# Kernel optimization log

Hardware: AMD Instinct MI355X
Metric: run time of the kernel (lower is better)

Reference implementation:

```python
import jax, jax.numpy as jnp
import numpy as np

N_NODES = 100000
N_EDGES = 1600000
D_IN = 128
H1 = 128           # hidden_channels
H2 = int(H1 * 0.6) # 76, per int(hidden_channels * 0.6)
D_OUT = 64


def setup_inputs() -> dict:
    key = jax.random.key(0)
    ks = jax.random.split(key, 12)
    def lin(k, fan_in, fan_out):
        # torch Linear default init: U(-1/sqrt(fan_in), 1/sqrt(fan_in)); stored as [in, out]
        bound = 1.0 / np.sqrt(fan_in)
        return jax.random.uniform(k, (fan_in, fan_out), jnp.float32, -bound, bound)
    x = jax.random.normal(ks[0], (N_NODES, D_IN), jnp.float32)
    edge_index = jax.random.randint(ks[1], (2, N_EDGES), 0, N_NODES, dtype=jnp.int64)
    return {
        "x": x,
        "edge_index": edge_index,
        "Wl1": lin(ks[2], D_IN, H1),  "Wr1": lin(ks[3], D_IN, H1),
        "b1": jnp.zeros((H1,), jnp.float32),
        "Wl2": lin(ks[4], H1, H2),    "Wr2": lin(ks[5], H1, H2),
        "b2": jnp.zeros((H2,), jnp.float32),
        "Wl3": lin(ks[6], H2, D_OUT), "Wr3": lin(ks[7], H2, D_OUT),
        "b3": jnp.zeros((D_OUT,), jnp.float32),
    }


def reference(x, edge_index, Wl1, Wr1, b1, Wl2, Wr2, b2, Wl3, Wr3, b3):
    src, dst = edge_index[0], edge_index[1]
    n = x.shape[0]
    # in-degree of each target node (mean aggregation denominator), clamped to 1
    deg = jax.ops.segment_sum(jnp.ones_like(src, dtype=x.dtype), dst, num_segments=n)
    inv_deg = (1.0 / jnp.maximum(deg, 1.0))[:, None]

    def sage(h, Wl, Wr, b):
        # gather source features, scatter-add to targets, mean, then dual linear
        agg = jax.ops.segment_sum(h[src], dst, num_segments=n) * inv_deg
        return agg @ Wl + h @ Wr + b  # lin_l(mean_j x_j) + lin_r(x_i) + bias

    h = jax.nn.relu(sage(x, Wl1, Wr1, b1))
    h = jax.nn.relu(sage(h, Wl2, Wr2, b2))
    return sage(h, Wl3, Wr3, b3)
```

## Files before the change

### kernel.cpp

```cpp
#include <hip/hip_runtime.h>
#include <hip/hip_bf16.h>
#include <cstdint>
#include <cstddef>


typedef __attribute__((ext_vector_type(8))) short bf16x8;
typedef __attribute__((ext_vector_type(4))) float f32x4;

__device__ __forceinline__ short f2bf(float f) {
  uint32_t u = __builtin_bit_cast(uint32_t, f);
  u += 0x7fffu + ((u >> 16) & 1u);
  return (short)(u >> 16);
}
__device__ __forceinline__ float bflo(uint32_t u) {
  union { uint32_t i; float f; } v; v.i = u << 16; return v.f;
}
__device__ __forceinline__ float bfhi(uint32_t u) {
  union { uint32_t i; float f; } v; v.i = u & 0xffff0000u; return v.f;
}
__device__ __forceinline__ uint32_t pkbf(float a, float b) {
  return (uint32_t)(uint16_t)f2bf(a) | ((uint32_t)(uint16_t)f2bf(b) << 16);
}

__global__ void k_detect(const int* __restrict__ ei, int* __restrict__ flag, int E) {
  int t = threadIdx.x;
  int stride = E / 4096; if (stride < 1) stride = 1;
  int found = 0;
  for (int i = t; i < 4096; i += 256) {
    long long e = (long long)i * stride;
    if (e < E && ei[2 * e + 1] != 0) found = 1;
  }
  if (found) atomicOr(flag, 1);
}

__device__ __forceinline__ int edge_val(const int* ei, int is64, size_t pos) {
  return is64 ? ei[2 * pos] : ei[pos];
}

#define GPART 256

__global__ __launch_bounds__(256)
void k_bhist(const int* __restrict__ ei, const int* __restrict__ flag,
             int* __restrict__ hist, int E, int NB, int CPB) {
  __shared__ int lh[1024];
  int g = blockIdx.x, t = threadIdx.x;
  for (int b = t; b < NB; b += 256) lh[b] = 0;
  __syncthreads();
  int is64 = (*flag == 0);
  int e0 = g * CPB, e1 = min(e0 + CPB, E);
  for (int e = e0 + t; e < e1; e += 256) {
    int d = edge_val(ei, is64, (size_t)E + e);
    atomicAdd(&lh[d >> 7], 1);
  }
  __syncthreads();
  for (int b = t; b < NB; b += 256) hist[(size_t)g * NB + b] = lh[b];
}

__global__ void k_csum(const int* __restrict__ hist, int* __restrict__ total,
                       int NB, int G) {
  int b = blockIdx.x, t = threadIdx.x;
  int s = 0;
  for (int g = t; g < G; g += 64) s += hist[(size_t)g * NB + b];
  for (int off = 32; off; off >>= 1) s += __shfl_down(s, off);
  if (t == 0) total[b] = s;
}

__global__ void k_bscan(const int* __restrict__ total, int* __restrict__ bbase,
                        int NB) {
  __shared__ int sh[1024];
  int t = threadIdx.x;
  int v = (t < NB) ? total[t] : 0;
  sh[t] = v; __syncthreads();
  for (int off = 1; off < 1024; off <<= 1) {
    int x = (t >= off) ? sh[t - off] : 0;
    __syncthreads();
    sh[t] += x;
    __syncthreads();
  }
  if (t < NB) bbase[t] = sh[t] - v;
  if (t == NB - 1) bbase[NB] = sh[t];
}

__global__ void k_coff(int* __restrict__ hist, const int* __restrict__ bbase,
                       int NB, int G) {
  int b = blockIdx.x, t = threadIdx.x;
  int carry = bbase[b];
  for (int g0 = 0; g0 < G; g0 += 64) {
    int v = hist[(size_t)(g0 + t) * NB + b];
    int incl = v;
    #pragma unroll
    for (int off = 1; off < 64; off <<= 1) {
      int x = __shfl_up(incl, off);
      if (t >= off) incl += x;
    }
    hist[(size_t)(g0 + t) * NB + b] = carry + incl - v;
    carry += __shfl(incl, 63);
  }
}

__global__ __launch_bounds__(256)
void k_bscatter(const int* __restrict__ ei, const int* __restrict__ flag,
                const int* __restrict__ off, uint32_t* __restrict__ staging,
                int E, int NB, int CPB) {
  __shared__ int lcur[1024];
  int g = blockIdx.x, t = threadIdx.x;
  for (int b = t; b < NB; b += 256) lcur[b] = off[(size_t)g * NB + b];
  __syncthreads();
  int is64 = (*flag == 0);
  int e0 = g * CPB, e1 = min(e0 + CPB, E);
  for (int e = e0 + t; e < e1; e += 256) {
    int s = edge_val(ei, is64, (size_t)e);
    int d = edge_val(ei, is64, (size_t)E + e);
    int p = atomicAdd(&lcur[d >> 7], 1);
    staging[p] = ((uint32_t)(d & 127) << 25) | (uint32_t)s;
  }
}

#define LDSCAP 12288
__global__ __launch_bounds__(256)
void k_bfinal(const uint32_t* __restrict__ staging, const int* __restrict__ bbase,
              int* __restrict__ row_start, int* __restrict__ sorted_src,
              int N, int NB, int E) {
  __shared__ uint32_t ent[LDSCAP];
  __shared__ int cnt[128];
  __shared__ int pre[128];
  int b = blockIdx.x, t = threadIdx.x;
  int base = bbase[b], sz = bbase[b + 1] - base;
  int n0 = b << 7;
  if (t < 128) cnt[t] = 0;
  __syncthreads();
  bool fit = (sz <= LDSCAP);
  if (fit) {
    for (int i = t; i < sz; i += 256) {
      uint32_t u = staging[base + i];
      ent[i] = u;
      atomicAdd(&cnt[u >> 25], 1);
    }
  } else {
    for (int i = t; i < sz; i += 256)
      atomicAdd(&cnt[staging[base + i] >> 25], 1);
  }
  __syncthreads();
  if (t < 128) pre[t] = cnt[t];
  __syncthreads();
  #pragma unroll
  for (int off = 1; off < 128; off <<= 1) {
    int x = (t < 128 && t >= off) ? pre[t - off] : 0;
    __syncthreads();
    if (t < 128) pre[t] += x;
    __syncthreads();
  }
  int nn = N - n0; if (nn > 128) nn = 128;
  if (t < 128) {
    int ex = pre[t] - cnt[t];
    if (t < nn) row_start[n0 + t] = base + ex;
    cnt[t] = ex;
  }
  if (b == NB - 1 && t == 0) row_start[N] = E;
  __syncthreads();
  if (fit) {
    for (int i = t; i < sz; i += 256) {
      uint32_t u = ent[i];
      int p = atomicAdd(&cnt[u >> 25], 1);
      sorted_src[base + p] = (int)(u & 0x1FFFFFFu);
    }
  } else {
    for (int i = t; i < sz; i += 256) {
      uint32_t u = staging[base + i];
      int p = atomicAdd(&cnt[u >> 25], 1);
      sorted_src[base + p] = (int)(u & 0x1FFFFFFu);
    }
  }
}

__global__ void k_wprep(const float* __restrict__ Wl, const float* __restrict__ Wr,
                        short* __restrict__ Wt, int K, int H, int Hp, int Kp, int NP) {
  int idx = blockIdx.x * 256 + threadIdx.x;
  if (idx >= NP * Kp) return;
  int c = idx / Kp, k = idx - c * Kp;
  float v = 0.f;
  if (k < K) {
    if (c < H) v = Wl[(size_t)k * H + c];
    else if (c >= Hp && c - Hp < H) v = Wr[(size_t)k * H + (c - Hp)];
  }
  Wt[idx] = f2bf(v);
}

template<int MODE, int NKS, int QBF16, int MAXCF>
__global__ __launch_bounds__(256, 3)
void k_gemm3(const void* __restrict__ Av, const short* __restrict__ Wt,
             const float* __restrict__ bias, short* __restrict__ P,
             void* __restrict__ Qv, int M, int lda, int H, int Hp, int F) {
  constexpr int Kp = NKS * 32;
  constexpr int PKv = Kp + 8;
  __shared__ short As[64 * PKv];
  int t = threadIdx.x;
  int wv = __builtin_amdgcn_readfirstlane(t >> 6);
  int lane = t & 63;
  int l16 = lane & 15, lk8 = (lane >> 4) * 8;
  int m0 = blockIdx.x * 64;

  if (MODE == 0) {
    const float* A = (const float*)Av;
    #pragma unroll
    for (int i = 0; i < 8; i++) {
      int c = t + i * 256;
      int row = c >> 5, q = c & 31;
      int gr = m0 + row;
      float4 v = make_float4(0.f, 0.f, 0.f, 0.f);
      if (gr < M) v = *(const float4*)(A + (size_t)gr * lda + q * 4);
      uint2 pk; pk.x = pkbf(v.x, v.y); pk.y = pkbf(v.z, v.w);
      *(uint2*)&As[row * PKv + q * 4] = pk;
    }
  } else {
    const short* A = (const short*)Av;
    constexpr int cpr = Kp / 8;
    #pragma unroll
    for (int i = 0; i < (64 * cpr) / 256; i++) {
      int c = t + i * 256;
      int row = c / cpr, q = c - row * cpr;
      int gr = m0 + row;
      uint4 v = make_uint4(0u, 0u, 0u, 0u);
      if (gr < M) v = *(const uint4*)(A + (size_t)gr * lda + q * 8);
      *(uint4*)&As[row * PKv + q * 8] = v;
    }
  }

  bf16x8 b[MAXCF][NKS];
  float4 bia[MAXCF];
  int cbase[MAXCF];
  bool isPc[MAXCF];
  bool cok[MAXCF];
  bool fragUse[MAXCF];
  #pragma unroll
  for (int i = 0; i < MAXCF; i++) {
    int cfrag = wv + 4 * i;
    fragUse[i] = cfrag < F;
    bool p = cfrag * 16 < Hp;
    int cb = cfrag * 16 + ((lane >> 4) << 2) - (p ? 0 : Hp);
    cbase[i] = cb; isPc[i] = p;
    cok[i] = fragUse[i] && (cb < H);
    bia[i] = make_float4(0.f, 0.f, 0.f, 0.f);
    if (cok[i] && !p) bia[i] = *(const float4*)(bias + cb);
    if (fragUse[i]) {
      const short* wp = Wt + (size_t)(cfrag * 16 + l16) * Kp + lk8;
      #pragma unroll
      for (int ks = 0; ks < NKS; ks++)
        b[i][ks] = *(const bf16x8*)(wp + ks * 32);
    } else {
      #pragma unroll
      for (int ks = 0; ks < NKS; ks++)
        b[i][ks] = (bf16x8){0, 0, 0, 0, 0, 0, 0, 0};
    }
  }

  __syncthreads();

  #pragma unroll
  for (int rf = 0; rf < 4; rf++) {
    bf16x8 a[NKS];
    #pragma unroll
    for (int ks = 0; ks < NKS; ks++)
      a[ks] = *(const bf16x8*)&As[(rf * 16 + l16) * PKv + ks * 32 + lk8];

    f32x4 acc[MAXCF];
    #pragma unroll
    for (int i = 0; i < MAXCF; i++) acc[i] = (f32x4){0.f, 0.f, 0.f, 0.f};
    #pragma unroll
    for (int ks = 0; ks < NKS; ks++) {
      #pragma unroll
      for (int i = 0; i < MAXCF; i++) {
        if (fragUse[i])
          acc[i] = __builtin_amdgcn_mfma_f32_16x16x32_bf16(b[i][ks], a[ks], acc[i], 0, 0, 0);
      }
    }

    int node = m0 + rf * 16 + l16;
    if (node < M) {
      #pragma unroll
      for (int i = 0; i < MAXCF; i++) {
        if (cok[i]) {
          if (isPc[i]) {
            uint2 pk;
            pk.x = pkbf(acc[i][0], acc[i][1]);
            pk.y = pkbf(acc[i][2], acc[i][3]);
            *(uint2*)(P + (size_t)node * H + cbase[i]) = pk;
          } else if (QBF16) {
            uint2 pk;
            pk.x = pkbf(acc[i][0] + bia[i].x, acc[i][1] + bia[i].y);
            pk.y = pkbf(acc[i][2] + bia[i].z, acc[i][3] + bia[i].w);
            *(uint2*)((short*)Qv + (size_t)node * H + cbase[i]) = pk;
          } else {
            float4 r;
            r.x = acc[i][0] + bia[i].x; r.y = acc[i][1] + bia[i].y;
            r.z = acc[i][2] + bia[i].z; r.w = acc[i][3] + bia[i].w;
            *(float4*)((float*)Qv + (size_t)node * H + cbase[i]) = r;
          }
        }
      }
    }
  }
}

template<int RELU, int PACK, int OUTBF16, int QBF16>
__global__ __launch_bounds__(256)
void k_agg(const short* __restrict__ P, const void* Q,
           const int* __restrict__ rs, const int* __restrict__ srcs,
           void* out, int N, int H, int HSo) {
  int wave = threadIdx.x >> 6;
  int lane = threadIdx.x & 63;
  int node = blockIdx.x * 4 + wave;
  if (node >= N) return;
  int start = rs[node];
  int deg = rs[node + 1] - start;
  int c = lane * PACK;
  bool act = c < H;
  float a0 = 0.f, a1 = 0.f;
  const int* sp = srcs + start;

  for (int base = 0; base < deg; base += 64) {
    int cnt = deg - base; if (cnt > 64) cnt = 64;
    int myidx = (lane < cnt) ? sp[base + lane] : 0;
    int e = 0;
    int nfull = cnt & ~3;
    for (; e < nfull; e += 4) {
      int s0 = __shfl(myidx, e);
      int s1 = __shfl(myidx, e + 1);
      int s2 = __shfl(myidx, e + 2);
      int s3 = __shfl(myidx, e + 3);
      if (act) {
        if (PACK == 2) {
          uint32_t u0 = *(const uint32_t*)(P + (size_t)s0 * H + c);
          uint32_t u1 = *(const uint32_t*)(P + (size_t)s1 * H + c);
          uint32_t u2 = *(const uint32_t*)(P + (size_t)s2 * H + c);
          uint32_t u3 = *(const uint32_t*)(P + (size_t)s3 * H + c);
          a0 += bflo(u0); a1 += bfhi(u0);
          a0 += bflo(u1); a1 += bfhi(u1);
          a0 += bflo(u2); a1 += bfhi(u2);
          a0 += bflo(u3); a1 += bfhi(u3);
        } else {
          uint32_t u0 = *(const uint16_t*)(P + (size_t)s0 * H + c);
          uint32_t u1 = *(const uint16_t*)(P + (size_t)s1 * H + c);
          uint32_t u2 = *(const uint16_t*)(P + (size_t)s2 * H + c);
          uint32_t u3 = *(const uint16_t*)(P + (size_t)s3 * H + c);
          a0 += bflo(u0) + bflo(u1) + bflo(u2) + bflo(u3);
        }
      }
    }
    for (; e < cnt; ++e) {
      int s0 = __shfl(myidx, e);
      if (act) {
        if (PACK == 2) {
          uint32_t u0 = *(const uint32_t*)(P + (size_t)s0 * H + c);
          a0 += bflo(u0); a1 += bfhi(u0);
        } else {
          uint32_t u0 = *(const uint16_t*)(P + (size_t)s0 * H + c);
          a0 += bflo(u0);
        }
      }
    }
  }

  if (!act) return;
  float scale = 1.f / (float)(deg > 0 ? deg : 1);
  size_t oq = (size_t)node * H + c;
  size_t oo = (size_t)node * HSo + c;
  if (PACK == 2) {
    float q0, q1;
    if (QBF16) {
      uint32_t qu = *(const uint32_t*)((const short*)Q + oq);
      q0 = bflo(qu); q1 = bfhi(qu);
    } else {
      float2 q = *(const float2*)((const float*)Q + oq);
      q0 = q.x; q1 = q.y;
    }
    float v0 = a0 * scale + q0;
    float v1 = a1 * scale + q1;
    if (RELU) { v0 = fmaxf(v0, 0.f); v1 = fmaxf(v1, 0.f); }
    if (OUTBF16) {
      *(uint32_t*)((short*)out + oo) = pkbf(v0, v1);
    } else {
      float2 r; r.x = v0; r.y = v1;
      *(float2*)((float*)out + oo) = r;
    }
  } else {
    float q0;
    if (QBF16) q0 = bflo(*(const uint16_t*)((const short*)Q + oq));
    else       q0 = ((const float*)Q)[oq];
    float v0 = a0 * scale + q0;
    if (RELU) v0 = fmaxf(v0, 0.f);
    if (OUTBF16) ((short*)out)[oo] = f2bf(v0);
    else ((float*)out)[oo] = v0;
  }
}

extern "C" void kernel_launch(void* const* d_in, const int* in_sizes, int n_in,
                              void* d_out, int out_size, void* d_ws, size_t ws_size,
                              hipStream_t stream) {
  const float* x   = (const float*)d_in[0];
  const int*   ei  = (const int*)d_in[1];
  const float* Wl1 = (const float*)d_in[2];
  const float* Wr1 = (const float*)d_in[3];
  const float* b1  = (const float*)d_in[4];
  const float* Wl2 = (const float*)d_in[5];
  const float* Wr2 = (const float*)d_in[6];
  const float* b2  = (const float*)d_in[7];
  const float* Wl3 = (const float*)d_in[8];
  const float* Wr3 = (const float*)d_in[9];
  const float* b3  = (const float*)d_in[10];

  const int DIN = 128;
  const int N  = in_sizes[0] / DIN;
  const int E  = in_sizes[1] / 2;
  const int H1 = in_sizes[4];
  const int H2 = in_sizes[7];
  const int H3 = in_sizes[10];
  const int Hp1 = 128, Hp2 = 80, Hp3 = 64;
  const int Kp12 = 128, Kp3 = 96;
  const int NB = (N + 127) >> 7;
  const int G = GPART;
  const int CPB = (E + G - 1) / G;

  char* w = (char*)d_ws;
  auto alloc = [&](size_t bytes) {
    char* p = w;
    w += (bytes + 255) & ~(size_t)255;
    return p;
  };
  short* bufP  = (short*)alloc((size_t)N * 128 * 2);
  short* bufH1 = (short*)alloc((size_t)N * 128 * 2);
  short* bufH2 = (short*)alloc((size_t)N * 96 * 2);
  short* q1    = (short*)alloc((size_t)N * 128 * 2);
  short* q2    = (short*)alloc((size_t)N * 76 * 2);
  float* q3    = (float*)alloc((size_t)N * 64 * 4);
  short* Wt1   = (short*)alloc((size_t)256 * 128 * 2);
  short* Wt2   = (short*)alloc((size_t)160 * 128 * 2);
  short* Wt3   = (short*)alloc((size_t)128 * 96 * 2);
  int* row_start = (int*)alloc((size_t)(N + 1) * 4);
  int* hist      = (int*)alloc((size_t)G * NB * 4);
  int* total     = (int*)alloc((size_t)NB * 4);
  int* bbase     = (int*)alloc((size_t)(NB + 1) * 4);
  uint32_t* staging = (uint32_t*)alloc((size_t)E * 4);
  int* sorted    = (int*)alloc((size_t)E * 4);
  int* flag      = (int*)alloc(256);

  k_wprep<<<(256 * 128 + 255) / 256, 256, 0, stream>>>(Wl1, Wr1, Wt1, DIN, H1, Hp1, Kp12, 2 * Hp1);
  k_wprep<<<(160 * 128 + 255) / 256, 256, 0, stream>>>(Wl2, Wr2, Wt2, H1, H2, Hp2, Kp12, 2 * Hp2);
  k_wprep<<<(128 * 96 + 255) / 256, 256, 0, stream>>>(Wl3, Wr3, Wt3, H2, H3, Hp3, Kp3, 2 * Hp3);

  hipMemsetAsync(flag, 0, 4, stream);
  k_detect<<<1, 256, 0, stream>>>(ei, flag, E);
  k_bhist<<<G, 256, 0, stream>>>(ei, flag, hist, E, NB, CPB);
  k_csum<<<NB, 64, 0, stream>>>(hist, total, NB, G);
  k_bscan<<<1, 1024, 0, stream>>>(total, bbase, NB);
  k_coff<<<NB, 64, 0, stream>>>(hist, bbase, NB, G);
  k_bscatter<<<G, 256, 0, stream>>>(ei, flag, hist, staging, E, NB, CPB);
  k_bfinal<<<NB, 256, 0, stream>>>(staging, bbase, row_start, sorted, N, NB, E);

  int gx = (N + 63) / 64;
  int aggGrid = (N + 3) / 4;

  k_gemm3<0, 4, 1, 4><<<gx, 256, 0, stream>>>(x, Wt1, b1, bufP, q1, N, DIN, H1, Hp1, 16);
  k_agg<1, 2, 1, 1><<<aggGrid, 256, 0, stream>>>(bufP, q1, row_start, sorted, bufH1, N, H1, 128);

  k_gemm3<1, 4, 1, 3><<<gx, 256, 0, stream>>>(bufH1, Wt2, b2, bufP, q2, N, Kp12, H2, Hp2, 10);
  k_agg<1, 2, 1, 1><<<aggGrid, 256, 0, stream>>>(bufP, q2, row_start, sorted, bufH2, N, H2, 96);

  k_gemm3<1, 3, 0, 2><<<gx, 256, 0, stream>>>(bufH2, Wt3, b3, bufP, q3, N, Kp3, H3, Hp3, 8);
  k_agg<0, 1, 0, 0><<<aggGrid, 256, 0, stream>>>(bufP, q3, row_start, sorted, d_out, N, H3, 64);
}
```

Before: 368.4 us.

## Enlarge GEMM row tile, swizzle LDS layout and pre-fragment weights

The dense transform GEMM now handles 128 rows per block instead of 64, so each block reuses its register-held weight fragments over twice as many rows. The A-tile in LDS uses an XOR swizzle in place of padding, and the weights are pre-packed into MFMA fragment order so each lane reads one contiguous 16-byte chunk. Column fragments are split among waves in contiguous ranges. The costs are a larger LDS footprint (32 KB) and half as many blocks, which could reduce occupancy and load balance.

New measurement: 378.1 us. +2.6%, slower.

```diff
diff --git a/kernel.cpp b/kernel.cpp
--- a/kernel.cpp
+++ b/kernel.cpp
@@ -174,57 +174,71 @@
 }
 
 __global__ void k_wprep(const float* __restrict__ Wl, const float* __restrict__ Wr,
-                        short* __restrict__ Wt, int K, int H, int Hp, int Kp, int NP) {
+                        short* __restrict__ WtF, int K, int H, int Hp,
+                        int NKS, int F) {
   int idx = blockIdx.x * 256 + threadIdx.x;
-  if (idx >= NP * Kp) return;
-  int c = idx / Kp, k = idx - c * Kp;
+  int total = F * NKS * 512;
+  if (idx >= total) return;
+  int j = idx & 7;
+  int lane = (idx >> 3) & 63;
+  int ks = (idx >> 9) % NKS;
+  int f = idx / (NKS * 512);
+  int c = f * 16 + (lane & 15);
+  int k = ks * 32 + (lane >> 4) * 8 + j;
   float v = 0.f;
   if (k < K) {
-    if (c < H) v = Wl[(size_t)k * H + c];
-    else if (c >= Hp && c - Hp < H) v = Wr[(size_t)k * H + (c - Hp)];
-  }
-  Wt[idx] = f2bf(v);
+    if (c < Hp) { if (c < H) v = Wl[(size_t)k * H + c]; }
+    else { int cc = c - Hp; if (cc < H) v = Wr[(size_t)k * H + cc]; }
+  }
+  WtF[idx] = f2bf(v);
 }
 
 template<int MODE, int NKS, int QBF16, int MAXCF>
 __global__ __launch_bounds__(256, 3)
-void k_gemm3(const void* __restrict__ Av, const short* __restrict__ Wt,
+void k_gemm4(const void* __restrict__ Av, const short* __restrict__ WtF,
              const float* __restrict__ bias, short* __restrict__ P,
              void* __restrict__ Qv, int M, int lda, int H, int Hp, int F) {
   constexpr int Kp = NKS * 32;
-  constexpr int PKv = Kp + 8;
-  __shared__ short As[64 * PKv];
+  __shared__ short As[128 * 128];
   int t = threadIdx.x;
   int wv = __builtin_amdgcn_readfirstlane(t >> 6);
   int lane = t & 63;
-  int l16 = lane & 15, lk8 = (lane >> 4) * 8;
-  int m0 = blockIdx.x * 64;
+  int l16 = lane & 15, kg = lane >> 4;
+  int m0 = blockIdx.x * 128;
 
   if (MODE == 0) {
     const float* A = (const float*)Av;
     #pragma unroll
-    for (int i = 0; i < 8; i++) {
+    for (int i = 0; i < 16; i++) {
       int c = t + i * 256;
       int row = c >> 5, q = c & 31;
       int gr = m0 + row;
       float4 v = make_float4(0.f, 0.f, 0.f, 0.f);
       if (gr < M) v = *(const float4*)(A + (size_t)gr * lda + q * 4);
       uint2 pk; pk.x = pkbf(v.x, v.y); pk.y = pkbf(v.z, v.w);
-      *(uint2*)&As[row * PKv + q * 4] = pk;
+      int bo = row * 256 + ((q * 8) ^ ((row & 7) << 4));
+      *(uint2*)((char*)As + bo) = pk;
     }
   } else {
     const short* A = (const short*)Av;
     constexpr int cpr = Kp / 8;
-    #pragma unroll
-    for (int i = 0; i < (64 * cpr) / 256; i++) {
+    constexpr int TOT = 128 * cpr;
+    #pragma unroll
+    for (int i = 0; i < (TOT + 255) / 256; i++) {
       int c = t + i * 256;
+      if ((TOT & 255) != 0 && c >= TOT) break;
       int row = c / cpr, q = c - row * cpr;
       int gr = m0 + row;
       uint4 v = make_uint4(0u, 0u, 0u, 0u);
       if (gr < M) v = *(const uint4*)(A + (size_t)gr * lda + q * 8);
-      *(uint4*)&As[row * PKv + q * 8] = v;
-    }
-  }
+      int bo = row * 256 + ((q * 16) ^ ((row & 7) << 4));
+      *(uint4*)((char*)As + bo) = v;
+    }
+  }
+
+  int qd = F >> 2, rm = F & 3;
+  int cf0 = wv * qd + (wv < rm ? wv : rm);
+  int myn = qd + (wv < rm ? 1 : 0);
 
   bf16x8 b[MAXCF][NKS];
   float4 bia[MAXCF];
@@ -234,19 +248,18 @@
   bool fragUse[MAXCF];
   #pragma unroll
   for (int i = 0; i < MAXCF; i++) {
-    int cfrag = wv + 4 * i;
-    fragUse[i] = cfrag < F;
-    bool p = cfrag * 16 < Hp;
-    int cb = cfrag * 16 + ((lane >> 4) << 2) - (p ? 0 : Hp);
+    int f = cf0 + i;
+    fragUse[i] = i < myn;
+    bool p = f * 16 < Hp;
+    int cb = f * 16 + (kg << 2) - (p ? 0 : Hp);
     cbase[i] = cb; isPc[i] = p;
     cok[i] = fragUse[i] && (cb < H);
     bia[i] = make_float4(0.f, 0.f, 0.f, 0.f);
     if (cok[i] && !p) bia[i] = *(const float4*)(bias + cb);
     if (fragUse[i]) {
-      const short* wp = Wt + (size_t)(cfrag * 16 + l16) * Kp + lk8;
       #pragma unroll
       for (int ks = 0; ks < NKS; ks++)
-        b[i][ks] = *(const bf16x8*)(wp + ks * 32);
+        b[i][ks] = *(const bf16x8*)(WtF + ((size_t)(f * NKS + ks) * 64 + lane) * 8);
     } else {
       #pragma unroll
       for (int ks = 0; ks < NKS; ks++)
@@ -257,11 +270,14 @@
   __syncthreads();
 
   #pragma unroll
-  for (int rf = 0; rf < 4; rf++) {
+  for (int rf = 0; rf < 8; rf++) {
+    int row = rf * 16 + l16;
     bf16x8 a[NKS];
     #pragma unroll
-    for (int ks = 0; ks < NKS; ks++)
-      a[ks] = *(const bf16x8*)&As[(rf * 16 + l16) * PKv + ks * 32 + lk8];
+    for (int ks = 0; ks < NKS; ks++) {
+      int bo = row * 256 + ((ks * 64 + kg * 16) ^ ((row & 7) << 4));
+      a[ks] = *(const bf16x8*)((const char*)As + bo);
+    }
 
     f32x4 acc[MAXCF];
     #pragma unroll
@@ -275,7 +291,7 @@
       }
     }
 
-    int node = m0 + rf * 16 + l16;
+    int node = m0 + row;
     if (node < M) {
       #pragma unroll
       for (int i = 0; i < MAXCF; i++) {
@@ -416,7 +432,6 @@
   const int H2 = in_sizes[7];
   const int H3 = in_sizes[10];
   const int Hp1 = 128, Hp2 = 80, Hp3 = 64;
-  const int Kp12 = 128, Kp3 = 96;
   const int NB = (N + 127) >> 7;
   const int G = GPART;
   const int CPB = (E + G - 1) / G;
@@ -433,9 +448,9 @@
   short* q1    = (short*)alloc((size_t)N * 128 * 2);
   short* q2    = (short*)alloc((size_t)N * 76 * 2);
   float* q3    = (float*)alloc((size_t)N * 64 * 4);
-  short* Wt1   = (short*)alloc((size_t)256 * 128 * 2);
-  short* Wt2   = (short*)alloc((size_t)160 * 128 * 2);
-  short* Wt3   = (short*)alloc((size_t)128 * 96 * 2);
+  short* Wt1   = (short*)alloc((size_t)16 * 4 * 512 * 2);
+  short* Wt2   = (short*)alloc((size_t)10 * 4 * 512 * 2);
+  short* Wt3   = (short*)alloc((size_t)8  * 3 * 512 * 2);
   int* row_start = (int*)alloc((size_t)(N + 1) * 4);
   int* hist      = (int*)alloc((size_t)G * NB * 4);
   int* total     = (int*)alloc((size_t)NB * 4);
@@ -444,9 +459,9 @@
   int* sorted    = (int*)alloc((size_t)E * 4);
   int* flag      = (int*)alloc(256);
 
-  k_wprep<<<(256 * 128 + 255) / 256, 256, 0, stream>>>(Wl1, Wr1, Wt1, DIN, H1, Hp1, Kp12, 2 * Hp1);
-  k_wprep<<<(160 * 128 + 255) / 256, 256, 0, stream>>>(Wl2, Wr2, Wt2, H1, H2, Hp2, Kp12, 2 * Hp2);
-  k_wprep<<<(128 * 96 + 255) / 256, 256, 0, stream>>>(Wl3, Wr3, Wt3, H2, H3, Hp3, Kp3, 2 * Hp3);
+  k_wprep<<<(16 * 4 * 512 + 255) / 256, 256, 0, stream>>>(Wl1, Wr1, Wt1, DIN, H1, Hp1, 4, 16);
+  k_wprep<<<(10 * 4 * 512 + 255) / 256, 256, 0, stream>>>(Wl2, Wr2, Wt2, H1, H2, Hp2, 4, 10);
+  k_wprep<<<(8  * 3 * 512 + 255) / 256, 256, 0, stream>>>(Wl3, Wr3, Wt3, H2, H3, Hp3, 3, 8);
 
   hipMemsetAsync(flag, 0, 4, stream);
   k_detect<<<1, 256, 0, stream>>>(ei, flag, E);
@@ -457,15 +472,15 @@
   k_bscatter<<<G, 256, 0, stream>>>(ei, flag, hist, staging, E, NB, CPB);
   k_bfinal<<<NB, 256, 0, stream>>>(staging, bbase, row_start, sorted, N, NB, E);
 
-  int gx = (N + 63) / 64;
+  int gx = (N + 127) / 128;
   int aggGrid = (N + 3) / 4;
 
-  k_gemm3<0, 4, 1, 4><<<gx, 256, 0, stream>>>(x, Wt1, b1, bufP, q1, N, DIN, H1, Hp1, 16);
+  k_gemm4<0, 4, 1, 4><<<gx, 256, 0, stream>>>(x, Wt1, b1, bufP, q1, N, DIN, H1, Hp1, 16);
   k_agg<1, 2, 1, 1><<<aggGrid, 256, 0, stream>>>(bufP, q1, row_start, sorted, bufH1, N, H1, 128);
 
-  k_gemm3<1, 4, 1, 3><<<gx, 256, 0, stream>>>(bufH1, Wt2, b2, bufP, q2, N, Kp12, H2, Hp2, 10);
+  k_gemm4<1, 4, 1, 3><<<gx, 256, 0, stream>>>(bufH1, Wt2, b2, bufP, q2, N, 128, H2, Hp2, 10);
   k_agg<1, 2, 1, 1><<<aggGrid, 256, 0, stream>>>(bufP, q2, row_start, sorted, bufH2, N, H2, 96);
 
-  k_gemm3<1, 3, 0, 2><<<gx, 256, 0, stream>>>(bufH2, Wt3, b3, bufP, q3, N, Kp3, H3, Hp3, 8);
+  k_gemm4<1, 3, 0, 2><<<gx, 256, 0, stream>>>(bufH2, Wt3, b3, bufP, q3, N, 96, H3, Hp3, 8);
   k_agg<0, 1, 0, 0><<<aggGrid, 256, 0, stream>>>(bufP, q3, row_start, sorted, d_out, N, H3, 64);
 }
```
